# Kernel tuning notes

Hardware: AMD Instinct MI355X
Metric: run time of the kernel (lower is better)

The kernel has to match this reference:

```python
import jax, jax.numpy as jnp
import numpy as np

VOCAB = 101
EMB = 32
HID = 32


def setup_inputs() -> dict:
    key = jax.random.key(0)
    k = jax.random.split(key, 7)
    B, T = 4096, 512
    x = jax.random.randint(k[0], (B, T), 0, VOCAB, dtype=jnp.int32)
    emb = jax.random.normal(k[1], (VOCAB, EMB), dtype=jnp.float32) * 0.1
    # gate order: i, f, g, o (concatenated along last dim)
    Wx = jax.random.normal(k[2], (EMB, 4 * HID), dtype=jnp.float32) * 0.1
    Wh = jax.random.normal(k[3], (HID, 4 * HID), dtype=jnp.float32) * 0.1
    b = jax.random.normal(k[4], (4 * HID,), dtype=jnp.float32) * 0.1
    W_fc = jax.random.normal(k[5], (HID, 2), dtype=jnp.float32) * 0.1
    b_fc = jax.random.normal(k[6], (2,), dtype=jnp.float32) * 0.1
    return {"x": x, "emb": emb, "Wx": Wx, "Wh": Wh, "b": b, "W_fc": W_fc, "b_fc": b_fc}


def _lstm_last_h(xe, Wx, Wh, b):
    # xe: [B, T, EMB]
    B = xe.shape[0]
    # precompute input contributions for all timesteps: [T, B, 4H]
    xg = jnp.einsum('bte,eh->tbh', xe, Wx) + b
    h0 = jnp.zeros((B, HID), xe.dtype)
    c0 = jnp.zeros((B, HID), xe.dtype)

    def step(carry, xt):
        h, c = carry
        g = xt + h @ Wh  # [B, 4H]
        i, f, gg, o = jnp.split(g, 4, axis=-1)
        c = jax.nn.sigmoid(f) * c + jax.nn.sigmoid(i) * jnp.tanh(gg)
        h = jax.nn.sigmoid(o) * jnp.tanh(c)
        return (h, c), None

    (h, c), _ = jax.lax.scan(step, (h0, c0), xg)
    return h  # last hidden state == hidden_seq[:, -1, :]


def reference(x, emb, Wx, Wh, b, W_fc, b_fc):
    xe = emb[x]  # [B, T, EMB]
    h = _lstm_last_h(xe, Wx, Wh, b)
    return h @ W_fc + b_fc  # [B, 2]
```

## Files before the change

kernel.cpp:

```cpp
#include <hip/hip_runtime.h>
#include <stdint.h>

#define T_LEN 512
#define VOCAB 101
#define GSP   136
#define XPB   516
#define HPW   20
#define HB1   (16 * HPW)

typedef short short8 __attribute__((ext_vector_type(8)));
typedef float f32x4  __attribute__((ext_vector_type(4)));

#define LOG2E 1.442695041f
#define L2E2  2.885390082f

__device__ __forceinline__ float asF(uint32_t u) {
    union { uint32_t i; float f; } x; x.i = u; return x.f;
}
__device__ __forceinline__ float bf2f(uint16_t u) { return asF(((uint32_t)u) << 16); }
__device__ __forceinline__ float bf_lo(uint32_t u) { return asF(u << 16); }
__device__ __forceinline__ float bf_hi(uint32_t u) { return asF(u & 0xFFFF0000u); }
__device__ __forceinline__ uint16_t f2bf(float f) {
    union { float f; uint32_t i; } x; x.f = f;
    return (uint16_t)((x.i + 0x7FFFu + ((x.i >> 16) & 1u)) >> 16);
}
__device__ __forceinline__ float getw(const void* p, int i, bool isbf) {
    return isbf ? bf2f(((const uint16_t*)p)[i]) : ((const float*)p)[i];
}
__device__ __forceinline__ bool detect_bf16(const void* embp) {
    const uint16_t* u = (const uint16_t*)embp;
    int sane = 0;
    for (int i = 0; i < 64; ++i) {
        uint16_t v = u[i];
        int e = (v >> 7) & 0xFF;
        sane += ((e >= 100 && e <= 140) || ((v & 0x7FFFu) == 0)) ? 1 : 0;
    }
    return sane >= 56;
}

#define GATES(S, CST, HOUT)                                                     \
  {                                                                             \
    float ai = __builtin_amdgcn_exp2f(-(S)[0]);                                 \
    float af = __builtin_amdgcn_exp2f(-(S)[1]);                                 \
    float ag = __builtin_amdgcn_exp2f(-(S)[2]);                                 \
    float ao = __builtin_amdgcn_exp2f(-(S)[3]);                                 \
    float uu = 1.f + ai, ww = 1.f + ag, zz = 1.f + af;                          \
    float uw = uu * ww;                                                         \
    float num = __builtin_fmaf(__builtin_fmaf(ww, -L2E2, 2.f * L2E2), zz,       \
                               (CST) * uw);                                     \
    float cs = num * __builtin_amdgcn_rcpf(zz * uw);                            \
    (CST) = cs;                                                                 \
    float ac = __builtin_amdgcn_exp2f(-cs);                                     \
    float t1 = 1.f + ac;                                                        \
    (HOUT) = (2.f - t1) * __builtin_amdgcn_rcpf((1.f + ao) * t1);               \
  }

#define STEP_T(HRoff, HWoff, TOFF, TKUSE, TKDEF)                                    \
  {                                                                                 \
    const uint32_t* hr = &hbuf[HRoff];                                              \
    uint32_t*       hw = &hbuf[HWoff];                                              \
    short8 bfrag = *(const short8*)&hr[n * HPW + 4 * q];                            \
    short8 graw  = *(const short8*)&Gl2[adr1 + (u0i << 2)];                         \
    TKDEF = xr[TOFF];                                                               \
    __builtin_amdgcn_sched_barrier(0);                                              \
    f32x4 gc0, gc1;                                                                 \
    { union { short8 v; uint32_t d[4]; } ug; ug.v = grawP;                          \
      gc0[0] = bf_lo(ug.d[0]); gc0[1] = bf_hi(ug.d[0]);                             \
      gc0[2] = bf_lo(ug.d[1]); gc0[3] = bf_hi(ug.d[1]);                             \
      gc1[0] = bf_lo(ug.d[2]); gc1[1] = bf_hi(ug.d[2]);                             \
      gc1[2] = bf_lo(ug.d[3]); gc1[3] = bf_hi(ug.d[3]); }                           \
    adr1 = (TKUSE) * GSP;                                                           \
    __builtin_amdgcn_sched_barrier(0);                                              \
    asm volatile("s_waitcnt lgkmcnt(2)" ::: "memory");                              \
    __builtin_amdgcn_sched_barrier(0);                                              \
    f32x4 s0 = __builtin_amdgcn_mfma_f32_16x16x32_bf16(afr0, bfrag, gc0, 0, 0, 0);  \
    f32x4 s1 = __builtin_amdgcn_mfma_f32_16x16x32_bf16(afr1, bfrag, gc1, 0, 0, 0);  \
    float h0, h1;                                                                   \
    GATES(s0, c0, h0);                                                              \
    GATES(s1, c1, h1);                                                              \
    uint32_t hp;                                                                    \
    asm("v_cvt_pk_bf16_f32 %0, %1, %2" : "=v"(hp) : "v"(h0), "v"(h1));              \
    hw[n * HPW + 4 * w + q] = hp;                                                   \
    grawP = graw;                                                                   \
    __builtin_amdgcn_sched_barrier(0);                                              \
    asm volatile("s_waitcnt lgkmcnt(0)" ::: "memory");                              \
    __builtin_amdgcn_s_barrier();                                                   \
    __builtin_amdgcn_sched_barrier(0);                                              \
  }

__global__ __launch_bounds__(256, 1) void lstm_fused(
    const int* __restrict__ x, const void* __restrict__ emb,
    const void* __restrict__ Wx, const void* __restrict__ Wh,
    const void* __restrict__ bias, const void* __restrict__ Wfc,
    const void* __restrict__ bfc, void* __restrict__ out)
{
    __shared__ __align__(16) uint16_t Gl2[VOCAB * GSP];
    __shared__ __align__(16) uint8_t  xt8[16 * XPB];
    __shared__ __align__(16) uint32_t hbuf[2 * 16 * HPW];

    const int tid = threadIdx.x;
    const int wl  = tid & 63;
    const int w   = tid >> 6;
    const int n   = wl & 15;
    const int q   = wl >> 4;
    const int b0  = blockIdx.x * 16;

    const bool isbf = detect_bf16(emb);

    for (int idx = tid; idx < VOCAB * 128; idx += 256) {
        int v = idx >> 7, cc = idx & 127;
        int u = cc >> 2, g = cc & 3;
        int col = 32 * g + u;
        float acc = getw(bias, col, isbf);
        #pragma unroll 8
        for (int k = 0; k < 32; ++k)
            acc += getw(emb, v * 32 + k, isbf) * getw(Wx, k * 128 + col, isbf);
        Gl2[v * GSP + cc] = f2bf(acc * ((g == 2) ? L2E2 : LOG2E));
    }
    for (int i = tid; i < 2048; i += 256) {
        int row = i >> 7, c4 = i & 127;
        int4 vv = *(const int4*)&x[(b0 + row) * T_LEN + (c4 << 2)];
        uint32_t p = (uint32_t)(vv.x & 255) | ((uint32_t)(vv.y & 255) << 8) |
                     ((uint32_t)(vv.z & 255) << 16) | ((uint32_t)(vv.w & 255) << 24);
        ((uint32_t*)&xt8[row * XPB])[c4] = p;
    }
    for (int i = tid; i < 48; i += 256) {
        int row = i / 3, j = i % 3;
        xt8[row * XPB + 512 + j] = (uint8_t)x[(b0 + row) * T_LEN + j];
    }
    for (int i = tid; i < 2 * 16 * HPW; i += 256) hbuf[i] = 0;

    short8 afr0, afr1;
    {
        const int gte = n & 3, ul = n >> 2;
        const float sc = (gte == 2) ? L2E2 : LOG2E;
        const int base = 32 * gte + 8 * w + 2 * ul;
        union { short8 v; uint16_t s[8]; } u0, u1;
        #pragma unroll
        for (int jj = 0; jj < 8; ++jj) {
            int kk = 8 * q + jj;
            u0.s[jj] = f2bf(getw(Wh, kk * 128 + base,     isbf) * sc);
            u1.s[jj] = f2bf(getw(Wh, kk * 128 + base + 1, isbf) * sc);
        }
        afr0 = u0.v; afr1 = u1.v;
    }
    __syncthreads();

    const int u0i = 8 * w + 2 * q;
    float c0 = 0.f, c1 = 0.f;
    const uint8_t* xr = &xt8[n * XPB];

    short8 grawP;
    int adr1, tkA, tkB;
    {
        int t0 = xr[0], t1 = xr[1];
        tkA = xr[2];
        grawP = *(const short8*)&Gl2[t0 * GSP + (u0i << 2)];
        adr1  = t1 * GSP;
    }

    for (int t = 0; t < T_LEN; t += 2) {
        STEP_T(0,   HB1, t + 3, tkA, tkB);
        STEP_T(HB1, 0,   t + 4, tkB, tkA);
    }

    __syncthreads();

    if (tid < 32) {
        int row = tid >> 1, cc = tid & 1;
        float acc = getw(bfc, cc, isbf);
        #pragma unroll 8
        for (int k = 0; k < 32; ++k) {
            uint32_t d = hbuf[row * HPW + (k >> 1)];
            float hval = (k & 1) ? bf_hi(d) : bf_lo(d);
            acc += hval * getw(Wfc, k * 2 + cc, isbf);
        }
        int oidx = (b0 + row) * 2 + cc;
        if (isbf) ((uint16_t*)out)[oidx] = f2bf(acc);
        else      ((float*)out)[oidx]    = acc;
    }
}

extern "C" void kernel_launch(void* const* d_in, const int* in_sizes, int n_in,
                              void* d_out, int out_size, void* d_ws, size_t ws_size,
                              hipStream_t stream) {
    (void)in_sizes; (void)n_in; (void)d_ws; (void)ws_size; (void)out_size;
    const int* x = (const int*)d_in[0];
    lstm_fused<<<dim3(256), dim3(256), 0, stream>>>(
        x, d_in[1], d_in[2], d_in[3], d_in[4], d_in[5], d_in[6], d_out);
}
```

Before: 288.0 us.

## Split hidden units across eight waves with one MFMA per wave per step

Doubles the block from four to eight wavefronts so each wave computes one 16x16 MFMA tile and one hidden unit per lane per timestep instead of two. Gate-input loads shrink to 4 bf16 values, h is written as 16-bit stores, and the Gl2 row pitch changes to keep alignment. The goal is to shorten the serial per-step critical path by halving the gate math per thread. In exchange, every timestep's block barrier now synchronises twice as many waves, which can add sync overhead.

```diff
diff --git a/kernel.cpp b/kernel.cpp
--- a/kernel.cpp
+++ b/kernel.cpp
@@ -3,12 +3,13 @@
 
 #define T_LEN 512
 #define VOCAB 101
-#define GSP   136
+#define GSP   140
 #define XPB   516
 #define HPW   20
 #define HB1   (16 * HPW)
 
 typedef short short8 __attribute__((ext_vector_type(8)));
+typedef short s16x4  __attribute__((ext_vector_type(4)));
 typedef float f32x4  __attribute__((ext_vector_type(4)));
 
 #define LOG2E 1.442695041f
@@ -58,29 +59,27 @@
 #define STEP_T(HRoff, HWoff, TOFF, TKUSE, TKDEF)                                    \
   {                                                                                 \
     const uint32_t* hr = &hbuf[HRoff];                                              \
-    uint32_t*       hw = &hbuf[HWoff];                                              \
+    uint16_t*       hw = (uint16_t*)&hbuf[HWoff];                                   \
     short8 bfrag = *(const short8*)&hr[n * HPW + 4 * q];                            \
-    short8 graw  = *(const short8*)&Gl2[adr1 + (u0i << 2)];                         \
+    __builtin_amdgcn_sched_barrier(0);                                              \
+    s16x4 graw  = *(const s16x4*)&Gl2[adr1 + (u4 << 2)];                            \
+    __builtin_amdgcn_sched_barrier(0);                                              \
     TKDEF = xr[TOFF];                                                               \
     __builtin_amdgcn_sched_barrier(0);                                              \
-    f32x4 gc0, gc1;                                                                 \
-    { union { short8 v; uint32_t d[4]; } ug; ug.v = grawP;                          \
-      gc0[0] = bf_lo(ug.d[0]); gc0[1] = bf_hi(ug.d[0]);                             \
-      gc0[2] = bf_lo(ug.d[1]); gc0[3] = bf_hi(ug.d[1]);                             \
-      gc1[0] = bf_lo(ug.d[2]); gc1[1] = bf_hi(ug.d[2]);                             \
-      gc1[2] = bf_lo(ug.d[3]); gc1[3] = bf_hi(ug.d[3]); }                           \
+    f32x4 gc;                                                                       \
+    { union { s16x4 v; uint32_t d[2]; } ug; ug.v = grawP;                           \
+      gc[0] = bf_lo(ug.d[0]); gc[1] = bf_hi(ug.d[0]);                               \
+      gc[2] = bf_lo(ug.d[1]); gc[3] = bf_hi(ug.d[1]); }                             \
     adr1 = (TKUSE) * GSP;                                                           \
     __builtin_amdgcn_sched_barrier(0);                                              \
     asm volatile("s_waitcnt lgkmcnt(2)" ::: "memory");                              \
     __builtin_amdgcn_sched_barrier(0);                                              \
-    f32x4 s0 = __builtin_amdgcn_mfma_f32_16x16x32_bf16(afr0, bfrag, gc0, 0, 0, 0);  \
-    f32x4 s1 = __builtin_amdgcn_mfma_f32_16x16x32_bf16(afr1, bfrag, gc1, 0, 0, 0);  \
-    float h0, h1;                                                                   \
+    f32x4 s0 = __builtin_amdgcn_mfma_f32_16x16x32_bf16(afr, bfrag, gc, 0, 0, 0);    \
+    float h0;                                                                       \
     GATES(s0, c0, h0);                                                              \
-    GATES(s1, c1, h1);                                                              \
     uint32_t hp;                                                                    \
-    asm("v_cvt_pk_bf16_f32 %0, %1, %2" : "=v"(hp) : "v"(h0), "v"(h1));              \
-    hw[n * HPW + 4 * w + q] = hp;                                                   \
+    asm("v_cvt_pk_bf16_f32 %0, %1, %2" : "=v"(hp) : "v"(h0), "v"(h0));              \
+    hw[n * (2 * HPW) + u4] = (uint16_t)hp;                                          \
     grawP = graw;                                                                   \
     __builtin_amdgcn_sched_barrier(0);                                              \
     asm volatile("s_waitcnt lgkmcnt(0)" ::: "memory");                              \
@@ -88,7 +87,7 @@
     __builtin_amdgcn_sched_barrier(0);                                              \
   }
 
-__global__ __launch_bounds__(256, 1) void lstm_fused(
+__global__ __launch_bounds__(512, 1) void lstm_fused(
     const int* __restrict__ x, const void* __restrict__ emb,
     const void* __restrict__ Wx, const void* __restrict__ Wh,
     const void* __restrict__ bias, const void* __restrict__ Wfc,
@@ -103,11 +102,12 @@
     const int w   = tid >> 6;
     const int n   = wl & 15;
     const int q   = wl >> 4;
+    const int u4  = 4 * w + q;
     const int b0  = blockIdx.x * 16;
 
     const bool isbf = detect_bf16(emb);
 
-    for (int idx = tid; idx < VOCAB * 128; idx += 256) {
+    for (int idx = tid; idx < VOCAB * 128; idx += 512) {
         int v = idx >> 7, cc = idx & 127;
         int u = cc >> 2, g = cc & 3;
         int col = 32 * g + u;
@@ -117,45 +117,41 @@
             acc += getw(emb, v * 32 + k, isbf) * getw(Wx, k * 128 + col, isbf);
         Gl2[v * GSP + cc] = f2bf(acc * ((g == 2) ? L2E2 : LOG2E));
     }
-    for (int i = tid; i < 2048; i += 256) {
+    for (int i = tid; i < 2048; i += 512) {
         int row = i >> 7, c4 = i & 127;
         int4 vv = *(const int4*)&x[(b0 + row) * T_LEN + (c4 << 2)];
         uint32_t p = (uint32_t)(vv.x & 255) | ((uint32_t)(vv.y & 255) << 8) |
                      ((uint32_t)(vv.z & 255) << 16) | ((uint32_t)(vv.w & 255) << 24);
         ((uint32_t*)&xt8[row * XPB])[c4] = p;
     }
-    for (int i = tid; i < 48; i += 256) {
+    for (int i = tid; i < 48; i += 512) {
         int row = i / 3, j = i % 3;
         xt8[row * XPB + 512 + j] = (uint8_t)x[(b0 + row) * T_LEN + j];
     }
-    for (int i = tid; i < 2 * 16 * HPW; i += 256) hbuf[i] = 0;
+    for (int i = tid; i < 2 * 16 * HPW; i += 512) hbuf[i] = 0;
 
-    short8 afr0, afr1;
+    short8 afr;
     {
         const int gte = n & 3, ul = n >> 2;
         const float sc = (gte == 2) ? L2E2 : LOG2E;
-        const int base = 32 * gte + 8 * w + 2 * ul;
-        union { short8 v; uint16_t s[8]; } u0, u1;
+        const int base = 32 * gte + 4 * w + ul;
+        union { short8 v; uint16_t s[8]; } u0;
         #pragma unroll
-        for (int jj = 0; jj < 8; ++jj) {
-            int kk = 8 * q + jj;
-            u0.s[jj] = f2bf(getw(Wh, kk * 128 + base,     isbf) * sc);
-            u1.s[jj] = f2bf(getw(Wh, kk * 128 + base + 1, isbf) * sc);
-        }
-        afr0 = u0.v; afr1 = u1.v;
+        for (int jj = 0; jj < 8; ++jj)
+            u0.s[jj] = f2bf(getw(Wh, (8 * q + jj) * 128 + base, isbf) * sc);
+        afr = u0.v;
     }
     __syncthreads();
 
-    const int u0i = 8 * w + 2 * q;
-    float c0 = 0.f, c1 = 0.f;
+    float c0 = 0.f;
     const uint8_t* xr = &xt8[n * XPB];
 
-    short8 grawP;
+    s16x4 grawP;
     int adr1, tkA, tkB;
     {
         int t0 = xr[0], t1 = xr[1];
         tkA = xr[2];
-        grawP = *(const short8*)&Gl2[t0 * GSP + (u0i << 2)];
+        grawP = *(const s16x4*)&Gl2[t0 * GSP + (u4 << 2)];
         adr1  = t1 * GSP;
     }
 
@@ -186,6 +182,6 @@
                               hipStream_t stream) {
     (void)in_sizes; (void)n_in; (void)d_ws; (void)ws_size; (void)out_size;
     const int* x = (const int*)d_in[0];
-    lstm_fused<<<dim3(256), dim3(256), 0, stream>>>(
+    lstm_fused<<<dim3(256), dim3(512), 0, stream>>>(
         x, d_in[1], d_in[2], d_in[3], d_in[4], d_in[5], d_in[6], d_out);
 }
```

New measurement: 245.4 us. -14.8%, faster.

## Halve sequences per block, duplicate rows in MFMA, run two blocks per CU

Applied to the files above, without the earlier changes.

Each block now handles 8 sequences instead of 16, and the grid doubles to 512 blocks with launch bounds allowing 2 blocks per CU. Each lane computes one hidden unit's gates instead of two, with the 16-wide MFMA N dimension filled by duplicating the 8 rows. The gate table is re-laid out with a new stride and odd blocks start slightly delayed. The aim is to shorten the per-step serial gate computation and overlap two independent recurrences per CU. The cost is redundant MFMA work and more total table-building work across blocks.

```diff
diff --git a/kernel.cpp b/kernel.cpp
--- a/kernel.cpp
+++ b/kernel.cpp
@@ -3,7 +3,7 @@
 
 #define T_LEN 512
 #define VOCAB 101
-#define GSP   136
+#define GSP   140
 #define XPB   516
 #define HPW   20
 #define HB1   (16 * HPW)
@@ -13,6 +13,7 @@
 
 #define LOG2E 1.442695041f
 #define L2E2  2.885390082f
+#define SB()  __builtin_amdgcn_sched_barrier(0)
 
 __device__ __forceinline__ float asF(uint32_t u) {
     union { uint32_t i; float f; } x; x.i = u; return x.f;
@@ -38,12 +39,12 @@
     return sane >= 56;
 }
 
-#define GATES(S, CST, HOUT)                                                     \
+#define GATES4(PI, PF, PG, PO, CST, HOUT)                                       \
   {                                                                             \
-    float ai = __builtin_amdgcn_exp2f(-(S)[0]);                                 \
-    float af = __builtin_amdgcn_exp2f(-(S)[1]);                                 \
-    float ag = __builtin_amdgcn_exp2f(-(S)[2]);                                 \
-    float ao = __builtin_amdgcn_exp2f(-(S)[3]);                                 \
+    float ai = __builtin_amdgcn_exp2f(-(PI));                                   \
+    float af = __builtin_amdgcn_exp2f(-(PF));                                   \
+    float ag = __builtin_amdgcn_exp2f(-(PG));                                   \
+    float ao = __builtin_amdgcn_exp2f(-(PO));                                   \
     float uu = 1.f + ai, ww = 1.f + ag, zz = 1.f + af;                          \
     float uw = uu * ww;                                                         \
     float num = __builtin_fmaf(__builtin_fmaf(ww, -L2E2, 2.f * L2E2), zz,       \
@@ -55,55 +56,64 @@
     (HOUT) = (2.f - t1) * __builtin_amdgcn_rcpf((1.f + ao) * t1);               \
   }
 
-#define STEP_T(HRoff, HWoff, TOFF, TKUSE, TKDEF)                                    \
+#define STEP_T(HRoff, HWoff, TOFF)                                                  \
   {                                                                                 \
     const uint32_t* hr = &hbuf[HRoff];                                              \
-    uint32_t*       hw = &hbuf[HWoff];                                              \
+    uint16_t*       hw = (uint16_t*)&hbuf[HWoff];                                   \
     short8 bfrag = *(const short8*)&hr[n * HPW + 4 * q];                            \
-    short8 graw  = *(const short8*)&Gl2[adr1 + (u0i << 2)];                         \
-    TKDEF = xr[TOFF];                                                               \
-    __builtin_amdgcn_sched_barrier(0);                                              \
+    SB();                                                                           \
+    short8 grN = *(const short8*)&Gl2[tokA * GSP + gofs];                           \
+    SB();                                                                           \
+    int tokN = xr[TOFF];                                                            \
+    SB();                                                                           \
     f32x4 gc0, gc1;                                                                 \
-    { union { short8 v; uint32_t d[4]; } ug; ug.v = grawP;                          \
+    { union { short8 v; uint32_t d[4]; } ug; ug.v = grC;                            \
       gc0[0] = bf_lo(ug.d[0]); gc0[1] = bf_hi(ug.d[0]);                             \
       gc0[2] = bf_lo(ug.d[1]); gc0[3] = bf_hi(ug.d[1]);                             \
       gc1[0] = bf_lo(ug.d[2]); gc1[1] = bf_hi(ug.d[2]);                             \
       gc1[2] = bf_lo(ug.d[3]); gc1[3] = bf_hi(ug.d[3]); }                           \
-    adr1 = (TKUSE) * GSP;                                                           \
-    __builtin_amdgcn_sched_barrier(0);                                              \
+    SB();                                                                           \
     asm volatile("s_waitcnt lgkmcnt(2)" ::: "memory");                              \
-    __builtin_amdgcn_sched_barrier(0);                                              \
+    SB();                                                                           \
     f32x4 s0 = __builtin_amdgcn_mfma_f32_16x16x32_bf16(afr0, bfrag, gc0, 0, 0, 0);  \
     f32x4 s1 = __builtin_amdgcn_mfma_f32_16x16x32_bf16(afr1, bfrag, gc1, 0, 0, 0);  \
-    float h0, h1;                                                                   \
-    GATES(s0, c0, h0);                                                              \
-    GATES(s1, c1, h1);                                                              \
+    float pi = hiN ? s1[0] : s0[0];                                                 \
+    float pf = hiN ? s1[1] : s0[1];                                                 \
+    float pg = hiN ? s1[2] : s0[2];                                                 \
+    float po = hiN ? s1[3] : s0[3];                                                 \
+    float h0;                                                                       \
+    GATES4(pi, pf, pg, po, c0, h0);                                                 \
     uint32_t hp;                                                                    \
-    asm("v_cvt_pk_bf16_f32 %0, %1, %2" : "=v"(hp) : "v"(h0), "v"(h1));              \
-    hw[n * HPW + 4 * w + q] = hp;                                                   \
-    grawP = graw;                                                                   \
-    __builtin_amdgcn_sched_barrier(0);                                              \
+    asm("v_cvt_pk_bf16_f32 %0, %1, %2" : "=v"(hp) : "v"(h0), "v"(h0));              \
+    hw[row * (2 * HPW) + uG]       = (uint16_t)hp;                                  \
+    hw[(row + 8) * (2 * HPW) + uG] = (uint16_t)hp;                                  \
+    grC = grN; tokA = tokN;                                                         \
+    SB();                                                                           \
     asm volatile("s_waitcnt lgkmcnt(0)" ::: "memory");                              \
     __builtin_amdgcn_s_barrier();                                                   \
-    __builtin_amdgcn_sched_barrier(0);                                              \
+    SB();                                                                           \
   }
 
-__global__ __launch_bounds__(256, 1) void lstm_fused(
+__global__ __launch_bounds__(256, 2) void lstm_fused(
     const int* __restrict__ x, const void* __restrict__ emb,
     const void* __restrict__ Wx, const void* __restrict__ Wh,
     const void* __restrict__ bias, const void* __restrict__ Wfc,
     const void* __restrict__ bfc, void* __restrict__ out)
 {
     __shared__ __align__(16) uint16_t Gl2[VOCAB * GSP];
-    __shared__ __align__(16) uint8_t  xt8[16 * XPB];
+    __shared__ __align__(16) uint8_t  xt8[8 * XPB];
     __shared__ __align__(16) uint32_t hbuf[2 * 16 * HPW];
 
     const int tid = threadIdx.x;
     const int wl  = tid & 63;
-    const int w   = tid >> 6;
+    const int wv  = tid >> 6;
     const int n   = wl & 15;
     const int q   = wl >> 4;
-    const int b0  = blockIdx.x * 16;
+    const int b0  = blockIdx.x * 8;
+    const bool hiN = ((n >> 3) & 1) != 0;
+    const int row = n & 7;
+    const int uG  = 8 * wv + q + (hiN ? 4 : 0);
+    const int gofs = wv * 32 + q * 8;
 
     const bool isbf = detect_bf16(emb);
 
@@ -115,18 +125,19 @@
         #pragma unroll 8
         for (int k = 0; k < 32; ++k)
             acc += getw(emb, v * 32 + k, isbf) * getw(Wx, k * 128 + col, isbf);
-        Gl2[v * GSP + cc] = f2bf(acc * ((g == 2) ? L2E2 : LOG2E));
-    }
-    for (int i = tid; i < 2048; i += 256) {
-        int row = i >> 7, c4 = i & 127;
-        int4 vv = *(const int4*)&x[(b0 + row) * T_LEN + (c4 << 2)];
+        int st = (u >> 3) * 32 + (u & 3) * 8 + ((u >> 2) & 1) * 4 + g;
+        Gl2[v * GSP + st] = f2bf(acc * ((g == 2) ? L2E2 : LOG2E));
+    }
+    for (int i = tid; i < 1024; i += 256) {
+        int r = i >> 7, c4 = i & 127;
+        int4 vv = *(const int4*)&x[(b0 + r) * T_LEN + (c4 << 2)];
         uint32_t p = (uint32_t)(vv.x & 255) | ((uint32_t)(vv.y & 255) << 8) |
                      ((uint32_t)(vv.z & 255) << 16) | ((uint32_t)(vv.w & 255) << 24);
-        ((uint32_t*)&xt8[row * XPB])[c4] = p;
-    }
-    for (int i = tid; i < 48; i += 256) {
-        int row = i / 3, j = i % 3;
-        xt8[row * XPB + 512 + j] = (uint8_t)x[(b0 + row) * T_LEN + j];
+        ((uint32_t*)&xt8[r * XPB])[c4] = p;
+    }
+    if (tid < 16) {
+        int r = tid >> 1, j = tid & 1;
+        xt8[r * XPB + 512 + j] = (uint8_t)x[(b0 + r) * T_LEN + j];
     }
     for (int i = tid; i < 2 * 16 * HPW; i += 256) hbuf[i] = 0;
 
@@ -134,48 +145,46 @@
     {
         const int gte = n & 3, ul = n >> 2;
         const float sc = (gte == 2) ? L2E2 : LOG2E;
-        const int base = 32 * gte + 8 * w + 2 * ul;
+        const int base = 32 * gte + 8 * wv + ul;
         union { short8 v; uint16_t s[8]; } u0, u1;
         #pragma unroll
         for (int jj = 0; jj < 8; ++jj) {
             int kk = 8 * q + jj;
             u0.s[jj] = f2bf(getw(Wh, kk * 128 + base,     isbf) * sc);
-            u1.s[jj] = f2bf(getw(Wh, kk * 128 + base + 1, isbf) * sc);
+            u1.s[jj] = f2bf(getw(Wh, kk * 128 + base + 4, isbf) * sc);
         }
         afr0 = u0.v; afr1 = u1.v;
     }
     __syncthreads();
-
-    const int u0i = 8 * w + 2 * q;
-    float c0 = 0.f, c1 = 0.f;
-    const uint8_t* xr = &xt8[n * XPB];
-
-    short8 grawP;
-    int adr1, tkA, tkB;
+    if (blockIdx.x & 1) __builtin_amdgcn_s_sleep(8);
+
+    const uint8_t* xr = &xt8[row * XPB];
+    float c0 = 0.f;
+    short8 grC;
+    int tokA;
     {
-        int t0 = xr[0], t1 = xr[1];
-        tkA = xr[2];
-        grawP = *(const short8*)&Gl2[t0 * GSP + (u0i << 2)];
-        adr1  = t1 * GSP;
+        int t0 = xr[0];
+        tokA = xr[1];
+        grC  = *(const short8*)&Gl2[t0 * GSP + gofs];
     }
 
     for (int t = 0; t < T_LEN; t += 2) {
-        STEP_T(0,   HB1, t + 3, tkA, tkB);
-        STEP_T(HB1, 0,   t + 4, tkB, tkA);
+        STEP_T(0,   HB1, t + 2);
+        STEP_T(HB1, 0,   t + 3);
     }
 
     __syncthreads();
 
-    if (tid < 32) {
-        int row = tid >> 1, cc = tid & 1;
+    if (tid < 16) {
+        int r = tid >> 1, cc = tid & 1;
         float acc = getw(bfc, cc, isbf);
         #pragma unroll 8
         for (int k = 0; k < 32; ++k) {
-            uint32_t d = hbuf[row * HPW + (k >> 1)];
+            uint32_t d = hbuf[r * HPW + (k >> 1)];
             float hval = (k & 1) ? bf_hi(d) : bf_lo(d);
             acc += hval * getw(Wfc, k * 2 + cc, isbf);
         }
-        int oidx = (b0 + row) * 2 + cc;
+        int oidx = (b0 + r) * 2 + cc;
         if (isbf) ((uint16_t*)out)[oidx] = f2bf(acc);
         else      ((float*)out)[oidx]    = acc;
     }
@@ -186,6 +195,6 @@
                               hipStream_t stream) {
     (void)in_sizes; (void)n_in; (void)d_ws; (void)ws_size; (void)out_size;
     const int* x = (const int*)d_in[0];
-    lstm_fused<<<dim3(256), dim3(256), 0, stream>>>(
+    lstm_fused<<<dim3(512), dim3(256), 0, stream>>>(
         x, d_in[1], d_in[2], d_in[3], d_in[4], d_in[5], d_in[6], d_out);
 }
```

Measured after the change: 326.4 us. 1.13x slower.
